# Optimization experiments

Hardware: AMD Instinct MI355X
Metric: run time of the kernel (lower is better)

Reference implementation:

```python
import jax, jax.numpy as jnp
import numpy as np

N_NODES = 50000
N_EDGES = 800000
IN_CH = 256
HID_CH = 128


def setup_inputs() -> dict:
    key = jax.random.key(0)
    k1, k2, k3, k4, k5 = jax.random.split(key, 5)
    x = jax.random.normal(k1, (N_NODES, IN_CH), dtype=jnp.float32)
    edge_index = jax.random.randint(k2, (2, N_EDGES), 0, N_NODES, dtype=jnp.int64)
    edge_weight = jax.random.uniform(k3, (N_EDGES,), dtype=jnp.float32)
    W = jax.random.normal(k4, (IN_CH, HID_CH), dtype=jnp.float32) * (1.0 / np.sqrt(IN_CH))
    b = jnp.zeros((HID_CH,), dtype=jnp.float32)
    alpha = jnp.full((HID_CH,), 0.25, dtype=jnp.float32)  # PReLU default init
    return {"x": x, "edge_index": edge_index, "edge_weight": edge_weight,
            "W": W, "b": b, "alpha": alpha}


def reference(x, edge_index, edge_weight, W, b, alpha):
    """GCNConv (with self-loops + symmetric normalization) followed by PReLU."""
    N = x.shape[0]
    row, col = edge_index[0], edge_index[1]
    # add self-loops with weight 1 (PyG gcn_norm default, add_self_loops=True)
    loop = jnp.arange(N, dtype=row.dtype)
    row = jnp.concatenate([row, loop])
    col = jnp.concatenate([col, loop])
    ew = jnp.concatenate([edge_weight, jnp.ones((N,), dtype=edge_weight.dtype)])
    # degree from edge weights, scattered at destination (col)
    deg = jax.ops.segment_sum(ew, col, num_segments=N)
    deg_inv_sqrt = jnp.where(deg > 0, jax.lax.rsqrt(deg), 0.0)
    norm = deg_inv_sqrt[row] * ew * deg_inv_sqrt[col]  # [E+N]
    # linear transform then gather-scale-scatter aggregation
    h = x @ W                               # [N, HID]
    msg = h[row] * norm[:, None]            # [E+N, HID]
    out = jax.ops.segment_sum(msg, col, num_segments=N) + b
    # PReLU with per-channel slope
    return jnp.where(out >= 0, out, alpha * out)
```

## Files before the change

### kernel.cpp

```cpp
#include <hip/hip_runtime.h>

#define NN 50000
#define NE 800000
#define KD 256
#define CD 128
#define NB 196
#define GEMM_BLOCKS 782
#define HIST_BLOCKS 3125
#define META_BLOCKS 782

typedef __attribute__((ext_vector_type(8))) short short8;
typedef __attribute__((ext_vector_type(4))) float floatx4;
typedef __attribute__((ext_vector_type(2))) float floatx2;

__device__ inline unsigned short f2bf(float f) {
    unsigned u = __float_as_uint(f);
    unsigned r = (u + 0x7FFFu + ((u >> 16) & 1u)) >> 16;
    return (unsigned short)r;
}
__device__ inline float bf2f_lo(unsigned u) { return __uint_as_float(u << 16); }
__device__ inline float bf2f_hi(unsigned u) { return __uint_as_float(u & 0xFFFF0000u); }

__global__ __launch_bounds__(256) void prep(const float* __restrict__ W,
                                            unsigned short* __restrict__ Wt,
                                            unsigned* __restrict__ packedAll,
                                            unsigned long long* __restrict__ state) {
    __shared__ unsigned short t[32][33];
    if (blockIdx.x < NB) {
        const int g = blockIdx.x * 256 + threadIdx.x;
        if (g < NN) {
#pragma unroll
            for (int c = 0; c < 4; c++) packedAll[(size_t)c * NN + g] = 0u;
        }
        if (blockIdx.x == 0) {
            for (int i = threadIdx.x; i < NB * 8; i += 256) state[i] = 0ull;
        }
        return;
    }
    const int b2 = blockIdx.x - NB;
    const int bk = (b2 & 7) * 32;
    const int bn = (b2 >> 3) * 32;
    const int tx = threadIdx.x & 31;
    const int ty = threadIdx.x >> 5;
#pragma unroll
    for (int i = 0; i < 32; i += 8)
        t[ty + i][tx] = f2bf(W[(size_t)(bk + ty + i) * CD + bn + tx]);
    __syncthreads();
#pragma unroll
    for (int i = 0; i < 32; i += 8)
        Wt[(size_t)(bn + ty + i) * KD + bk + tx] = t[tx][ty + i];
}

__global__ __launch_bounds__(256) void fused_gemm_hist(
        const float* __restrict__ x, const unsigned short* __restrict__ Wt,
        unsigned short* __restrict__ hb,
        const int* __restrict__ col, const float* __restrict__ ew,
        unsigned* __restrict__ packedAll, unsigned short* __restrict__ rank) {
    __shared__ unsigned short Bs[128][68];

    if (blockIdx.x >= GEMM_BLOCKS) {
        const int hblk = blockIdx.x - GEMM_BLOCKS;
        const int e = hblk * 256 + threadIdx.x;
        if (e < NE) {
            unsigned* packed = packedAll + (size_t)(hblk & 3) * NN;
            unsigned p = (1u << 24) + (unsigned)(ew[e] * 262144.0f);
            unsigned old = atomicAdd(&packed[col[e]], p);
            rank[e] = (unsigned short)(old >> 24);
        }
        return;
    }

    const int tid  = threadIdx.x;
    const int wave = tid >> 6;
    const int lane = tid & 63;
    const int row0 = blockIdx.x * 64;
    const int m0   = wave * 16;
    const int lr   = lane & 15;
    const int quad = lane >> 4;

    const int grow_a = row0 + m0 + lr;
    const bool ok = grow_a < NN;
    const float* xp = x + (size_t)grow_a * KD + quad * 8;

    union { short8 v; unsigned short us[8]; } avs[8];
#pragma unroll
    for (int kt = 0; kt < 8; kt++) {
        if (ok) {
            const float4 f0 = *(const float4*)(xp + kt * 32);
            const float4 f1 = *(const float4*)(xp + kt * 32 + 4);
            avs[kt].us[0] = f2bf(f0.x); avs[kt].us[1] = f2bf(f0.y);
            avs[kt].us[2] = f2bf(f0.z); avs[kt].us[3] = f2bf(f0.w);
            avs[kt].us[4] = f2bf(f1.x); avs[kt].us[5] = f2bf(f1.y);
            avs[kt].us[6] = f2bf(f1.z); avs[kt].us[7] = f2bf(f1.w);
        } else {
            avs[kt].v = (short8){0,0,0,0,0,0,0,0};
        }
    }

    floatx4 acc[8];
#pragma unroll
    for (int nt = 0; nt < 8; nt++) acc[nt] = (floatx4){0.f, 0.f, 0.f, 0.f};

#pragma unroll
    for (int kq = 0; kq < 4; kq++) {
        if (kq) __syncthreads();
#pragma unroll
        for (int r8 = 0; r8 < 4; r8++) {
            const int idx  = r8 * 256 + tid;
            const int rown = idx >> 3;
            const int koff = (idx & 7) * 8;
            *(short8*)&Bs[rown][koff] =
                *(const short8*)(Wt + (size_t)rown * KD + kq * 64 + koff);
        }
        __syncthreads();
#pragma unroll
        for (int kt2 = 0; kt2 < 2; kt2++) {
            const int kt = kq * 2 + kt2;
            short8 b[8];
#pragma unroll
            for (int nt = 0; nt < 8; nt++)
                b[nt] = *(const short8*)&Bs[nt * 16 + lr][kt2 * 32 + quad * 8];
#pragma unroll
            for (int nt = 0; nt < 8; nt++)
                acc[nt] = __builtin_amdgcn_mfma_f32_16x16x32_bf16(
                              avs[kt].v, b[nt], acc[nt], 0, 0, 0);
        }
    }

#pragma unroll
    for (int i = 0; i < 4; i++) {
        const int grow = row0 + m0 + quad * 4 + i;
        if (grow < NN) {
            unsigned short* hp = hb + (size_t)grow * CD + lr;
#pragma unroll
            for (int nt = 0; nt < 8; nt++)
                hp[nt * 16] = f2bf(acc[nt][i]);
        }
    }
}

__global__ __launch_bounds__(256) void scan_lookback(
        const unsigned* __restrict__ packedAll,
        unsigned long long* __restrict__ state,
        int* __restrict__ start, int4* __restrict__ base4,
        float* __restrict__ dinv) {
    __shared__ int sm[256];
    __shared__ int sbase;
    const int t = threadIdx.x;
    const int b = blockIdx.x;
    const int g = b * 256 + t;

    int cc[4] = {0, 0, 0, 0};
    unsigned lowsum = 0;
    int v = 0;
    if (g < NN) {
#pragma unroll
        for (int c = 0; c < 4; c++) {
            unsigned p = packedAll[(size_t)c * NN + g];
            cc[c] = (int)(p >> 24);
            lowsum += p & 0xFFFFFFu;
            v += cc[c];
        }
    }
    sm[t] = v;
    __syncthreads();
#pragma unroll
    for (int off = 1; off < 256; off <<= 1) {
        int u = (t >= off) ? sm[t - off] : 0;
        __syncthreads();
        sm[t] += u;
        __syncthreads();
    }
    const int incl = sm[t];
    const int total = sm[255];

    if (t == 0) {
        unsigned long long post =
            ((b == 0 ? 2ull : 1ull) << 32) | (unsigned)total;
        __hip_atomic_store(&state[(size_t)b * 8], post,
                           __ATOMIC_RELAXED, __HIP_MEMORY_SCOPE_AGENT);
        if (b == 0) sbase = 0;
    }
    if (b > 0 && t < 64) {
        long long run = 0;
        int i = b - 1;
        while (true) {
            const int idx = i - t;
            unsigned long long s = (idx >= 0)
                ? __hip_atomic_load(&state[(size_t)idx * 8],
                                    __ATOMIC_RELAXED, __HIP_MEMORY_SCOPE_AGENT)
                : (2ull << 32);
            const unsigned st = (unsigned)(s >> 32);
            const unsigned long long b0m = __ballot(st == 0u);
            const unsigned long long b2m = __ballot(st == 2u);
            if (b2m) {
                const int L = __ffsll((long long)b2m) - 1;
                const unsigned long long below =
                    (L == 63) ? ~0ull : ((1ull << (L + 1)) - 1ull);
                if (b0m & below) { __builtin_amdgcn_s_sleep(1); continue; }
                unsigned val = (t <= L) ? (unsigned)s : 0u;
#pragma unroll
                for (int o = 32; o; o >>= 1) val += __shfl_xor(val, o);
                run += val;
                break;
            } else if (b0m) {
                const int L0 = __ffsll((long long)b0m) - 1;
                unsigned val = (t < L0) ? (unsigned)s : 0u;
#pragma unroll
                for (int o = 32; o; o >>= 1) val += __shfl_xor(val, o);
                run += val;
                i -= L0;
                if (L0 == 0) __builtin_amdgcn_s_sleep(1);
            } else {
                unsigned val = (unsigned)s;
#pragma unroll
                for (int o = 32; o; o >>= 1) val += __shfl_xor(val, o);
                run += val;
                i -= 64;
            }
        }
        if (t == 0) {
            __hip_atomic_store(&state[(size_t)b * 8],
                               (2ull << 32) | (unsigned)(run + total),
                               __ATOMIC_RELAXED, __HIP_MEMORY_SCOPE_AGENT);
            sbase = (int)run;
        }
    }
    __syncthreads();
    const int base = sbase;

    if (g < NN) {
        const int s = base + (incl - v);
        start[g] = s;
        base4[g] = make_int4(s, s + cc[0], s + cc[0] + cc[1], s + cc[0] + cc[1] + cc[2]);
        float degs = (float)lowsum * (1.0f / 262144.0f);
        dinv[g] = rsqrtf(1.0f + degs);
    }
    if (g == 0) start[NN] = NE;
}

__global__ __launch_bounds__(256) void meta_write(const int* __restrict__ row,
                                                  const int* __restrict__ col,
                                                  const float* __restrict__ ew,
                                                  const unsigned short* __restrict__ rank,
                                                  const int4* __restrict__ base4,
                                                  const float* __restrict__ dinv,
                                                  unsigned* __restrict__ meta) {
    const int e0 = (blockIdx.x * 256 + threadIdx.x) * 4;
    if (e0 >= NE) return;
    const int4 c4 = *(const int4*)(col + e0);
    const int4 r4 = *(const int4*)(row + e0);
    const float4 w4 = *(const float4*)(ew + e0);
    const ushort4 k4 = *(const ushort4*)(rank + e0);
    const int cs[4] = {c4.x, c4.y, c4.z, c4.w};
    const int rs[4] = {r4.x, r4.y, r4.z, r4.w};
    const float wsv[4] = {w4.x, w4.y, w4.z, w4.w};
    const unsigned short ks[4] = {k4.x, k4.y, k4.z, k4.w};
#pragma unroll
    for (int j = 0; j < 4; j++) {
        const int e = e0 + j;
        const int copy = (e >> 8) & 3;
        const int4 b4 = base4[cs[j]];
        const int base = (copy == 0) ? b4.x : (copy == 1) ? b4.y
                       : (copy == 2) ? b4.z : b4.w;
        const unsigned short wbf = f2bf(dinv[rs[j]] * wsv[j]);
        meta[base + ks[j]] = ((unsigned)wbf << 16) | (unsigned)rs[j];
    }
}

__global__ __launch_bounds__(256) void aggregate(const int* __restrict__ start,
                                                 const unsigned* __restrict__ meta,
                                                 const unsigned short* __restrict__ hb,
                                                 const float* __restrict__ dinv,
                                                 const float* __restrict__ bias,
                                                 const float* __restrict__ alpha,
                                                 float* __restrict__ out) {
    int n = blockIdx.x * 4 + (threadIdx.x >> 6);
    if (n >= NN) return;
    n = __builtin_amdgcn_readfirstlane(n);
    const int lane = threadIdx.x & 63;
    const int s = __builtin_amdgcn_readfirstlane(start[n]);
    const int e = __builtin_amdgcn_readfirstlane(start[n + 1]);

    float A0[8], A1[8];
#pragma unroll
    for (int j = 0; j < 8; j++) { A0[j] = 0.f; A1[j] = 0.f; }

    int i = s;
    for (; i + 8 <= e; i += 8) {
        unsigned m[8], u[8];
#pragma unroll
        for (int j = 0; j < 8; j++) m[j] = __builtin_nontemporal_load(meta + i + j);
#pragma unroll
        for (int j = 0; j < 8; j++)
            u[j] = *(const unsigned*)(hb + (size_t)(m[j] & 0xFFFFu) * CD + lane * 2);
#pragma unroll
        for (int j = 0; j < 8; j++) {
            float w = __uint_as_float(m[j] & 0xFFFF0000u);
            A0[j] = fmaf(w, bf2f_lo(u[j]), A0[j]);
            A1[j] = fmaf(w, bf2f_hi(u[j]), A1[j]);
        }
    }
    for (; i < e; i++) {
        unsigned m = __builtin_nontemporal_load(meta + i);
        unsigned u = *(const unsigned*)(hb + (size_t)(m & 0xFFFFu) * CD + lane * 2);
        float w = __uint_as_float(m & 0xFFFF0000u);
        A0[0] = fmaf(w, bf2f_lo(u), A0[0]);
        A1[0] = fmaf(w, bf2f_hi(u), A1[0]);
    }
#pragma unroll
    for (int j = 1; j < 8; j++) { A0[0] += A0[j]; A1[0] += A1[j]; }

    const float dc = dinv[n];
    unsigned us = *(const unsigned*)(hb + (size_t)n * CD + lane * 2);
    const int ch = lane * 2;
    float o0 = dc * A0[0] + dc * dc * bf2f_lo(us) + bias[ch];
    float o1 = dc * A1[0] + dc * dc * bf2f_hi(us) + bias[ch + 1];
    o0 = o0 >= 0.f ? o0 : alpha[ch] * o0;
    o1 = o1 >= 0.f ? o1 : alpha[ch + 1] * o1;
    floatx2 o; o.x = o0; o.y = o1;
    __builtin_nontemporal_store(o, (floatx2*)(out + (size_t)n * CD + ch));
}

extern "C" void kernel_launch(void* const* d_in, const int* in_sizes, int n_in,
                              void* d_out, int out_size, void* d_ws, size_t ws_size,
                              hipStream_t stream) {
    const float* x     = (const float*)d_in[0];
    const int*   eidx  = (const int*)d_in[1];
    const float* ew    = (const float*)d_in[2];
    const float* Wm    = (const float*)d_in[3];
    const float* bias  = (const float*)d_in[4];
    const float* alpha = (const float*)d_in[5];
    const int* row = eidx;
    const int* col = eidx + NE;

    float* out = (float*)d_out;

    char* ws = (char*)d_ws;
    unsigned* packedAll = (unsigned*)(ws);
    int*   start    = (int*)(ws + 800000);
    float* dinv     = (float*)(ws + 1000064);
    unsigned short* rank = (unsigned short*)(ws + 1200064);
    int4*  base4    = (int4*)(ws + 2800064);
    unsigned* meta  = (unsigned*)(ws + 3600064);
    unsigned short* Wt = (unsigned short*)(ws + 6800064);
    unsigned long long* state = (unsigned long long*)(ws + 6865600);
    unsigned short* hb = (unsigned short*)(ws + 6878208);

    prep          <<<NB + 32, 256, 0, stream>>>(Wm, Wt, packedAll, state);
    fused_gemm_hist<<<GEMM_BLOCKS + HIST_BLOCKS, 256, 0, stream>>>(
                        x, Wt, hb, col, ew, packedAll, rank);
    scan_lookback <<<NB, 256, 0, stream>>>(packedAll, state, start, base4, dinv);
    meta_write    <<<META_BLOCKS, 256, 0, stream>>>(row, col, ew, rank, base4, dinv, meta);
    aggregate     <<<(NN + 3) / 4, 256, 0, stream>>>(start, meta, hb, dinv, bias, alpha, out);
}
```

Measured before the change: 188.3 us.

## Privatize degree histogram per XCD with workgroup-scope atomics

The edge-degree histogram now keeps one copy per XCD, picked from the hardware XCC_ID register, instead of four copies picked by block index. The atomics use workgroup scope, so each counter is only touched by one XCD and can stay in that XCD's L2 rather than going through device-coherent paths. The copy index is packed into the rank value. The scan and meta-write kernels now read and write an 8-entry per-node base array. The trade-off is more scan input and base-table traffic, and correctness now relies on the scope choice and on each copy staying under 256 edges per node.

```diff
diff --git a/kernel.cpp b/kernel.cpp
--- a/kernel.cpp
+++ b/kernel.cpp
@@ -8,6 +8,7 @@
 #define GEMM_BLOCKS 782
 #define HIST_BLOCKS 3125
 #define META_BLOCKS 782
+#define NCOPY 8
 
 typedef __attribute__((ext_vector_type(8))) short short8;
 typedef __attribute__((ext_vector_type(4))) float floatx4;
@@ -20,6 +21,12 @@
 }
 __device__ inline float bf2f_lo(unsigned u) { return __uint_as_float(u << 16); }
 __device__ inline float bf2f_hi(unsigned u) { return __uint_as_float(u & 0xFFFF0000u); }
+
+__device__ inline unsigned xcd_id() {
+    unsigned x;
+    asm volatile("s_getreg_b32 %0, hwreg(HW_REG_XCC_ID)" : "=s"(x));
+    return x & (NCOPY - 1);
+}
 
 __global__ __launch_bounds__(256) void prep(const float* __restrict__ W,
                                             unsigned short* __restrict__ Wt,
@@ -30,7 +37,7 @@
         const int g = blockIdx.x * 256 + threadIdx.x;
         if (g < NN) {
 #pragma unroll
-            for (int c = 0; c < 4; c++) packedAll[(size_t)c * NN + g] = 0u;
+            for (int c = 0; c < NCOPY; c++) packedAll[(size_t)c * NN + g] = 0u;
         }
         if (blockIdx.x == 0) {
             for (int i = threadIdx.x; i < NB * 8; i += 256) state[i] = 0ull;
@@ -62,10 +69,12 @@
         const int hblk = blockIdx.x - GEMM_BLOCKS;
         const int e = hblk * 256 + threadIdx.x;
         if (e < NE) {
-            unsigned* packed = packedAll + (size_t)(hblk & 3) * NN;
+            const unsigned copy = xcd_id();
+            unsigned* packed = packedAll + (size_t)copy * NN;
             unsigned p = (1u << 24) + (unsigned)(ew[e] * 262144.0f);
-            unsigned old = atomicAdd(&packed[col[e]], p);
-            rank[e] = (unsigned short)(old >> 24);
+            unsigned old = __hip_atomic_fetch_add(&packed[col[e]], p,
+                               __ATOMIC_RELAXED, __HIP_MEMORY_SCOPE_WORKGROUP);
+            rank[e] = (unsigned short)((copy << 8) | (old >> 24));
         }
         return;
     }
@@ -142,7 +151,7 @@
 __global__ __launch_bounds__(256) void scan_lookback(
         const unsigned* __restrict__ packedAll,
         unsigned long long* __restrict__ state,
-        int* __restrict__ start, int4* __restrict__ base4,
+        int* __restrict__ start, int* __restrict__ base8,
         float* __restrict__ dinv) {
     __shared__ int sm[256];
     __shared__ int sbase;
@@ -150,12 +159,14 @@
     const int b = blockIdx.x;
     const int g = b * 256 + t;
 
-    int cc[4] = {0, 0, 0, 0};
+    int cc[NCOPY];
     unsigned lowsum = 0;
     int v = 0;
+#pragma unroll
+    for (int c = 0; c < NCOPY; c++) cc[c] = 0;
     if (g < NN) {
 #pragma unroll
-        for (int c = 0; c < 4; c++) {
+        for (int c = 0; c < NCOPY; c++) {
             unsigned p = packedAll[(size_t)c * NN + g];
             cc[c] = (int)(p >> 24);
             lowsum += p & 0xFFFFFFu;
@@ -232,7 +243,12 @@
     if (g < NN) {
         const int s = base + (incl - v);
         start[g] = s;
-        base4[g] = make_int4(s, s + cc[0], s + cc[0] + cc[1], s + cc[0] + cc[1] + cc[2]);
+        int pfx = s;
+#pragma unroll
+        for (int j = 0; j < NCOPY; j++) {
+            base8[(size_t)g * NCOPY + j] = pfx;
+            pfx += cc[j];
+        }
         float degs = (float)lowsum * (1.0f / 262144.0f);
         dinv[g] = rsqrtf(1.0f + degs);
     }
@@ -243,7 +259,7 @@
                                                   const int* __restrict__ col,
                                                   const float* __restrict__ ew,
                                                   const unsigned short* __restrict__ rank,
-                                                  const int4* __restrict__ base4,
+                                                  const int* __restrict__ base8,
                                                   const float* __restrict__ dinv,
                                                   unsigned* __restrict__ meta) {
     const int e0 = (blockIdx.x * 256 + threadIdx.x) * 4;
@@ -258,13 +274,11 @@
     const unsigned short ks[4] = {k4.x, k4.y, k4.z, k4.w};
 #pragma unroll
     for (int j = 0; j < 4; j++) {
-        const int e = e0 + j;
-        const int copy = (e >> 8) & 3;
-        const int4 b4 = base4[cs[j]];
-        const int base = (copy == 0) ? b4.x : (copy == 1) ? b4.y
-                       : (copy == 2) ? b4.z : b4.w;
+        const int copy = ks[j] >> 8;
+        const int cnt  = ks[j] & 255;
+        const int base = base8[(size_t)cs[j] * NCOPY + copy];
         const unsigned short wbf = f2bf(dinv[rs[j]] * wsv[j]);
-        meta[base + ks[j]] = ((unsigned)wbf << 16) | (unsigned)rs[j];
+        meta[base + cnt] = ((unsigned)wbf << 16) | (unsigned)rs[j];
     }
 }
 
@@ -338,19 +352,19 @@
 
     char* ws = (char*)d_ws;
     unsigned* packedAll = (unsigned*)(ws);
-    int*   start    = (int*)(ws + 800000);
-    float* dinv     = (float*)(ws + 1000064);
-    unsigned short* rank = (unsigned short*)(ws + 1200064);
-    int4*  base4    = (int4*)(ws + 2800064);
-    unsigned* meta  = (unsigned*)(ws + 3600064);
-    unsigned short* Wt = (unsigned short*)(ws + 6800064);
-    unsigned long long* state = (unsigned long long*)(ws + 6865600);
-    unsigned short* hb = (unsigned short*)(ws + 6878208);
+    int*   start    = (int*)(ws + 1600000);
+    float* dinv     = (float*)(ws + 1800064);
+    unsigned short* rank = (unsigned short*)(ws + 2000064);
+    int*   base8    = (int*)(ws + 3600064);
+    unsigned* meta  = (unsigned*)(ws + 5200064);
+    unsigned short* Wt = (unsigned short*)(ws + 8400064);
+    unsigned long long* state = (unsigned long long*)(ws + 8465600);
+    unsigned short* hb = (unsigned short*)(ws + 8478208);
 
     prep          <<<NB + 32, 256, 0, stream>>>(Wm, Wt, packedAll, state);
     fused_gemm_hist<<<GEMM_BLOCKS + HIST_BLOCKS, 256, 0, stream>>>(
                         x, Wt, hb, col, ew, packedAll, rank);
-    scan_lookback <<<NB, 256, 0, stream>>>(packedAll, state, start, base4, dinv);
-    meta_write    <<<META_BLOCKS, 256, 0, stream>>>(row, col, ew, rank, base4, dinv, meta);
+    scan_lookback <<<NB, 256, 0, stream>>>(packedAll, state, start, base8, dinv);
+    meta_write    <<<META_BLOCKS, 256, 0, stream>>>(row, col, ew, rank, base8, dinv, meta);
     aggregate     <<<(NN + 3) / 4, 256, 0, stream>>>(start, meta, hb, dinv, bias, alpha, out);
 }
```

Result: no change. 187.7 us (-0.3%).

## Move edge histogram into prep kernel and zero counters with memset

Applied to the files above, without the earlier changes.

Splits the fused GEMM+histogram launch: the atomic degree/rank histogram now runs in the prep kernel alongside the W transpose, and the GEMM becomes its own kernel. The packed counters are cleared with hipMemsetAsync instead of dedicated prep blocks, and the state reset moves to the first transpose block. This reorders work across kernels, possibly to keep the atomic traffic from contending with the GEMM, but it adds a memset call and an extra kernel boundary.

```diff
diff --git a/kernel.cpp b/kernel.cpp
--- a/kernel.cpp
+++ b/kernel.cpp
@@ -21,23 +21,26 @@
 __device__ inline float bf2f_lo(unsigned u) { return __uint_as_float(u << 16); }
 __device__ inline float bf2f_hi(unsigned u) { return __uint_as_float(u & 0xFFFF0000u); }
 
-__global__ __launch_bounds__(256) void prep(const float* __restrict__ W,
-                                            unsigned short* __restrict__ Wt,
-                                            unsigned* __restrict__ packedAll,
-                                            unsigned long long* __restrict__ state) {
+__global__ __launch_bounds__(256) void hist_prep(
+        const float* __restrict__ W, unsigned short* __restrict__ Wt,
+        const int* __restrict__ col, const float* __restrict__ ew,
+        unsigned* __restrict__ packedAll, unsigned short* __restrict__ rank,
+        unsigned long long* __restrict__ state) {
     __shared__ unsigned short t[32][33];
-    if (blockIdx.x < NB) {
-        const int g = blockIdx.x * 256 + threadIdx.x;
-        if (g < NN) {
-#pragma unroll
-            for (int c = 0; c < 4; c++) packedAll[(size_t)c * NN + g] = 0u;
-        }
-        if (blockIdx.x == 0) {
-            for (int i = threadIdx.x; i < NB * 8; i += 256) state[i] = 0ull;
+    if (blockIdx.x < HIST_BLOCKS) {
+        const int e = blockIdx.x * 256 + threadIdx.x;
+        if (e < NE) {
+            unsigned* packed = packedAll + (size_t)(blockIdx.x & 3) * NN;
+            unsigned p = (1u << 24) + (unsigned)(ew[e] * 262144.0f);
+            unsigned old = atomicAdd(&packed[col[e]], p);
+            rank[e] = (unsigned short)(old >> 24);
         }
         return;
     }
-    const int b2 = blockIdx.x - NB;
+    const int b2 = blockIdx.x - HIST_BLOCKS;
+    if (b2 == 0) {
+        for (int i = threadIdx.x; i < NB * 8; i += 256) state[i] = 0ull;
+    }
     const int bk = (b2 & 7) * 32;
     const int bn = (b2 >> 3) * 32;
     const int tx = threadIdx.x & 31;
@@ -51,24 +54,10 @@
         Wt[(size_t)(bn + ty + i) * KD + bk + tx] = t[tx][ty + i];
 }
 
-__global__ __launch_bounds__(256) void fused_gemm_hist(
+__global__ __launch_bounds__(256) void gemm(
         const float* __restrict__ x, const unsigned short* __restrict__ Wt,
-        unsigned short* __restrict__ hb,
-        const int* __restrict__ col, const float* __restrict__ ew,
-        unsigned* __restrict__ packedAll, unsigned short* __restrict__ rank) {
+        unsigned short* __restrict__ hb) {
     __shared__ unsigned short Bs[128][68];
-
-    if (blockIdx.x >= GEMM_BLOCKS) {
-        const int hblk = blockIdx.x - GEMM_BLOCKS;
-        const int e = hblk * 256 + threadIdx.x;
-        if (e < NE) {
-            unsigned* packed = packedAll + (size_t)(hblk & 3) * NN;
-            unsigned p = (1u << 24) + (unsigned)(ew[e] * 262144.0f);
-            unsigned old = atomicAdd(&packed[col[e]], p);
-            rank[e] = (unsigned short)(old >> 24);
-        }
-        return;
-    }
 
     const int tid  = threadIdx.x;
     const int wave = tid >> 6;
@@ -338,19 +327,20 @@
 
     char* ws = (char*)d_ws;
     unsigned* packedAll = (unsigned*)(ws);
-    int*   start    = (int*)(ws + 800000);
-    float* dinv     = (float*)(ws + 1000064);
-    unsigned short* rank = (unsigned short*)(ws + 1200064);
-    int4*  base4    = (int4*)(ws + 2800064);
-    unsigned* meta  = (unsigned*)(ws + 3600064);
-    unsigned short* Wt = (unsigned short*)(ws + 6800064);
-    unsigned long long* state = (unsigned long long*)(ws + 6865600);
-    unsigned short* hb = (unsigned short*)(ws + 6878208);
-
-    prep          <<<NB + 32, 256, 0, stream>>>(Wm, Wt, packedAll, state);
-    fused_gemm_hist<<<GEMM_BLOCKS + HIST_BLOCKS, 256, 0, stream>>>(
-                        x, Wt, hb, col, ew, packedAll, rank);
-    scan_lookback <<<NB, 256, 0, stream>>>(packedAll, state, start, base4, dinv);
-    meta_write    <<<META_BLOCKS, 256, 0, stream>>>(row, col, ew, rank, base4, dinv, meta);
-    aggregate     <<<(NN + 3) / 4, 256, 0, stream>>>(start, meta, hb, dinv, bias, alpha, out);
-}
+    unsigned long long* state = (unsigned long long*)(ws + 800000);
+    int*   start    = (int*)(ws + 812544);
+    float* dinv     = (float*)(ws + 1012608);
+    unsigned short* rank = (unsigned short*)(ws + 1212608);
+    int4*  base4    = (int4*)(ws + 2812608);
+    unsigned* meta  = (unsigned*)(ws + 3612608);
+    unsigned short* Wt = (unsigned short*)(ws + 6812608);
+    unsigned short* hb = (unsigned short*)(ws + 6878144);
+
+    hipMemsetAsync(packedAll, 0, 800000, stream);
+    hist_prep    <<<HIST_BLOCKS + 32, 256, 0, stream>>>(Wm, Wt, col, ew,
+                                                        packedAll, rank, state);
+    gemm         <<<GEMM_BLOCKS, 256, 0, stream>>>(x, Wt, hb);
+    scan_lookback<<<NB, 256, 0, stream>>>(packedAll, state, start, base4, dinv);
+    meta_write   <<<META_BLOCKS, 256, 0, stream>>>(row, col, ew, rank, base4, dinv, meta);
+    aggregate    <<<(NN + 3) / 4, 256, 0, stream>>>(start, meta, hb, dinv, bias, alpha, out);
+}
```

Measured after the change: 205.4 us. 1.09x slower.
